# Kernel tuning notes

Measured on AMD Instinct MI355X. Metric: run time of the kernel, lower is better.

The kernel has to match this reference:

```python
import jax, jax.numpy as jnp
import numpy as np

D_MODEL = 1024
N_HEADS = 16
HEAD_DIM = D_MODEL // N_HEADS
D_FF = 4 * D_MODEL
SEQ = 2048
BATCH = 2
EPS = 1e-6


def setup_inputs() -> dict:
    key = jax.random.key(0)
    ks = jax.random.split(key, 8)
    s = 0.02
    return {
        "x": jax.random.normal(ks[0], (SEQ, BATCH, D_MODEL), dtype=jnp.float32),
        "g1": jnp.ones((D_MODEL,), dtype=jnp.float32),                # norm1 weight
        "g2": jnp.ones((D_MODEL,), dtype=jnp.float32),                # norm2 weight
        "Wq": jax.random.normal(ks[1], (N_HEADS, D_MODEL, HEAD_DIM), dtype=jnp.float32) * s,
        "Wk": jax.random.normal(ks[2], (N_HEADS, D_MODEL, HEAD_DIM), dtype=jnp.float32) * s,
        "Wv": jax.random.normal(ks[3], (N_HEADS, D_MODEL, HEAD_DIM), dtype=jnp.float32) * s,
        "Wo": jax.random.normal(ks[4], (D_MODEL, D_MODEL), dtype=jnp.float32) * s,
        "W1": jax.random.normal(ks[5], (D_MODEL, D_FF), dtype=jnp.float32) * s,
        "W2": jax.random.normal(ks[6], (D_FF, D_MODEL), dtype=jnp.float32) * s,
    }


def _rmsnorm(x, g):
    rms = jnp.sqrt(jnp.mean(x * x, axis=-1, keepdims=True) + EPS)
    return g * (x / rms)


def _block(x, g1, g2, Wq, Wk, Wv, Wo, W1, W2):
    S = x.shape[0]
    scale = HEAD_DIM ** -0.5
    # --- attention (pre-norm) ---
    h = _rmsnorm(x, g1)                              # (S, B, D)
    Q = jnp.einsum('sbd,hdk->bhsk', h, Wq)           # (B, H, S, K)
    K = jnp.einsum('sbd,hdk->bhsk', h, Wk)
    V = jnp.einsum('sbd,hdk->bhsk', h, Wv)
    scores = jnp.einsum('bhsk,bhtk->bhst', Q, K) * scale
    causal = jnp.tril(jnp.ones((S, S), dtype=bool))
    scores = jnp.where(causal, scores, -jnp.inf)
    attn = jax.nn.softmax(scores, axis=-1)
    ctx = jnp.einsum('bhst,bhtk->sbhk', attn, V)     # heads concatenated in order
    ctx = ctx.reshape(S, x.shape[1], D_MODEL)
    x = x + ctx @ Wo
    # --- FFN (pre-norm) ---
    h2 = _rmsnorm(x, g2)
    x = x + jax.nn.silu(h2 @ W1) @ W2
    return x


def reference(x, g1, g2, Wq, Wk, Wv, Wo, W1, W2):
    return _block(x, g1, g2, Wq, Wk, Wv, Wo, W1, W2)
```

## Files before the change

### kernel.cpp

```cpp
#include <hip/hip_runtime.h>

typedef unsigned short u16;
typedef __bf16 bf16x8 __attribute__((ext_vector_type(8)));
typedef u16 u16x8 __attribute__((ext_vector_type(8)));
typedef u16 u16x4 __attribute__((ext_vector_type(4)));
typedef float f32x4 __attribute__((ext_vector_type(4)));

__device__ __forceinline__ u16 f2bf(float f) {
    union { float f; unsigned int u; } x; x.f = f;
    unsigned int r = x.u + 0x7FFFu + ((x.u >> 16) & 1u);
    return (u16)(r >> 16);
}

__device__ __forceinline__ u16 f2bf_hw(float f) {
    union { __bf16 b; u16 u; } x; x.b = (__bf16)f; return x.u;
}

__device__ __forceinline__ void gload_lds16(const u16* g, u16* l) {
    __builtin_amdgcn_global_load_lds(
        (const __attribute__((address_space(1))) unsigned int*)g,
        (__attribute__((address_space(3))) unsigned int*)l, 16, 0, 0);
}


__global__ __launch_bounds__(256) void qkvT_k(
    const float* __restrict__ Wq, const float* __restrict__ Wk,
    const float* __restrict__ Wv, u16* __restrict__ out)
{
    __shared__ float T[64][65];
    const int d0 = blockIdx.x * 64;
    const int y = blockIdx.y;
    const int wsel = y >> 4, h = y & 15;
    const float* W = (wsel == 0) ? Wq : (wsel == 1) ? Wk : Wv;
    const float scale = (wsel == 0) ? 0.125f * 1.44269504088896f : 1.0f;
    const int tid = threadIdx.x;
    const int tr = tid >> 4;
    const int tc = (tid & 15) * 4;
    #pragma unroll
    for (int k = 0; k < 4; k++) {
        f32x4 v = *(const f32x4*)(W + (size_t)h * 65536 + (size_t)(d0 + 16 * k + tr) * 64 + tc);
        T[16 * k + tr][tc]     = v[0];
        T[16 * k + tr][tc + 1] = v[1];
        T[16 * k + tr][tc + 2] = v[2];
        T[16 * k + tr][tc + 3] = v[3];
    }
    __syncthreads();
    #pragma unroll
    for (int k = 0; k < 4; k++) {
        const int kk = 16 * k + tr;
        u16x4 o;
        #pragma unroll
        for (int i = 0; i < 4; i++) o[i] = f2bf(T[tc + i][kk] * scale);
        *(u16x4*)(out + (size_t)(wsel * 1024 + h * 64 + kk) * 1024 + d0 + tc) = o;
    }
}

__global__ __launch_bounds__(256) void transT_k(
    const float* __restrict__ in, u16* __restrict__ out, int R, int C)
{
    __shared__ float T[64][65];
    const int r0 = blockIdx.x * 64, c0 = blockIdx.y * 64;
    const int tid = threadIdx.x;
    const int tr = tid >> 4;
    const int tc = (tid & 15) * 4;
    #pragma unroll
    for (int k = 0; k < 4; k++) {
        f32x4 v = *(const f32x4*)(in + (size_t)(c0 + 16 * k + tr) * R + r0 + tc);
        T[16 * k + tr][tc]     = v[0];
        T[16 * k + tr][tc + 1] = v[1];
        T[16 * k + tr][tc + 2] = v[2];
        T[16 * k + tr][tc + 3] = v[3];
    }
    __syncthreads();
    #pragma unroll
    for (int k = 0; k < 4; k++) {
        const int rl = 16 * k + tr;
        u16x4 o;
        #pragma unroll
        for (int i = 0; i < 4; i++) o[i] = f2bf(T[tc + i][rl]);
        *(u16x4*)(out + (size_t)(r0 + rl) * C + c0 + tc) = o;
    }
}

__global__ __launch_bounds__(256) void vtrans_k(const u16* __restrict__ qkv, u16* __restrict__ vT)
{
    __shared__ u16 T[64][72];
    const int bh = blockIdx.x, b = bh >> 4, h = bh & 15;
    const int s0 = blockIdx.y * 64;
    const int tid = threadIdx.x;
    const int r = tid >> 2, c0 = (tid & 3) * 16;
    const u16* src = qkv + ((size_t)((s0 + r) * 2 + b)) * 3072 + 2048 + h * 64 + c0;
    *(u16x8*)&T[r][c0] = *(const u16x8*)src;
    *(u16x8*)&T[r][c0 + 8] = *(const u16x8*)(src + 8);
    __syncthreads();
    u16x8 o0, o1;
    #pragma unroll
    for (int i = 0; i < 8; i++) o0[i] = T[c0 + i][r];
    #pragma unroll
    for (int i = 0; i < 8; i++) o1[i] = T[c0 + 8 + i][r];
    u16* dst = vT + (size_t)(bh * 64 + r) * 2048 + s0 + c0;
    *(u16x8*)dst = o0;
    *(u16x8*)(dst + 8) = o1;
}

__global__ __launch_bounds__(256) void rmsnorm_k(
    const float* __restrict__ x, const float* __restrict__ g, u16* __restrict__ out)
{
    const int row = blockIdx.x;
    const int tid = threadIdx.x;
    const float* xr = x + (size_t)row * 1024;
    f32x4 v = *(const f32x4*)(xr + tid * 4);
    float ss = v[0] * v[0] + v[1] * v[1] + v[2] * v[2] + v[3] * v[3];
    #pragma unroll
    for (int off = 32; off > 0; off >>= 1) ss += __shfl_down(ss, off);
    __shared__ float red[4];
    if ((tid & 63) == 0) red[tid >> 6] = ss;
    __syncthreads();
    float sum = red[0] + red[1] + red[2] + red[3];
    float rinv = rsqrtf(sum * (1.0f / 1024.0f) + 1e-6f);
    f32x4 gv = *(const f32x4*)(g + tid * 4);
    u16x4 o;
    #pragma unroll
    for (int i = 0; i < 4; i++) o[i] = f2bf(v[i] * gv[i] * rinv);
    *(u16x4*)(out + (size_t)row * 1024 + tid * 4) = o;
}

__global__ __launch_bounds__(256) void addred_norm_k(
    const float* __restrict__ res, const float* __restrict__ p0,
    const float* __restrict__ p1, const float* __restrict__ g,
    float* __restrict__ xout, u16* __restrict__ hout)
{
    const int row = blockIdx.x;
    const int tid = threadIdx.x;
    const size_t base = (size_t)row * 1024 + tid * 4;
    f32x4 a = *(const f32x4*)(res + base);
    f32x4 b = *(const f32x4*)(p0 + base);
    f32x4 c = *(const f32x4*)(p1 + base);
    f32x4 o = a + b + c;
    *(f32x4*)(xout + base) = o;
    float ss = o[0] * o[0] + o[1] * o[1] + o[2] * o[2] + o[3] * o[3];
    #pragma unroll
    for (int off = 32; off > 0; off >>= 1) ss += __shfl_down(ss, off);
    __shared__ float red[4];
    if ((tid & 63) == 0) red[tid >> 6] = ss;
    __syncthreads();
    float sum = red[0] + red[1] + red[2] + red[3];
    float rinv = rsqrtf(sum * (1.0f / 1024.0f) + 1e-6f);
    f32x4 gv = *(const f32x4*)(g + tid * 4);
    u16x4 hv;
    #pragma unroll
    for (int i = 0; i < 4; i++) hv[i] = f2bf(o[i] * gv[i] * rinv);
    *(u16x4*)(hout + base) = hv;
}

__global__ __launch_bounds__(256) void addred_k(
    const float* __restrict__ res, const float* __restrict__ p0,
    const float* __restrict__ p1, float* __restrict__ out)
{
    int i = (blockIdx.x * 256 + threadIdx.x) * 4;
    f32x4 a = *(const f32x4*)(res + i);
    f32x4 b = *(const f32x4*)(p0 + i);
    f32x4 c = *(const f32x4*)(p1 + i);
    f32x4 o = a + b + c;
    *(f32x4*)(out + i) = o;
}

template <int MODE>
__global__ __launch_bounds__(256) void gemm_bt_k(
    const u16* __restrict__ A, const u16* __restrict__ BT,
    u16* __restrict__ outB, float* __restrict__ outF, const float* __restrict__ res,
    int M, int N, int K, int klen)
{
    __shared__ u16 As[128 * 64];
    __shared__ u16 Bs[128 * 64];
    const int tid = threadIdx.x;
    const int lane = tid & 63, w = tid >> 6;
    const int wm = w >> 1, wn = w & 1;
    const int quad = lane >> 4, l15 = lane & 15;
    const int bid = blockIdx.x + gridDim.x * blockIdx.y;
    const int bj = bid >> 3;
    const int m0 = ((bid & 7) * 4 + (bj & 3)) * 128;
    const int n0 = (bj >> 2) * 128;
    const int kbeg = blockIdx.z * klen;

    f32x4 acc[4][4] = {};

    const int srow = (w << 3) + (lane >> 3);
    const int swz = ((lane & 7) ^ (lane >> 3)) << 3;
    const u16* aA = A + (size_t)(m0 + srow) * K + kbeg + swz;
    const u16* aB = BT + (size_t)(n0 + srow) * K + kbeg + swz;
    u16* lA = As + w * 512;
    u16* lB = Bs + w * 512;
    const int rsw = (l15 & 7) << 3;

    for (int k0 = 0; k0 < klen; k0 += 64) {
        __syncthreads();
        #pragma unroll
        for (int c = 0; c < 4; c++)
            gload_lds16(aA + (size_t)(c * 32) * K + k0, lA + c * 2048);
        #pragma unroll
        for (int c = 0; c < 4; c++)
            gload_lds16(aB + (size_t)(c * 32) * K + k0, lB + c * 2048);
        __syncthreads();
        #pragma unroll
        for (int kh = 0; kh < 2; kh++) {
            const int cb = ((kh * 4 + quad) << 3);
            bf16x8 af[4], bfr[4];
            #pragma unroll
            for (int i = 0; i < 4; i++)
                af[i] = *(const bf16x8*)(As + (wm * 64 + i * 16 + l15) * 64 + (cb ^ rsw));
            #pragma unroll
            for (int j = 0; j < 4; j++)
                bfr[j] = *(const bf16x8*)(Bs + (wn * 64 + j * 16 + l15) * 64 + (cb ^ rsw));
            #pragma unroll
            for (int i = 0; i < 4; i++)
                #pragma unroll
                for (int j = 0; j < 4; j++)
                    acc[i][j] = __builtin_amdgcn_mfma_f32_16x16x32_bf16(af[i], bfr[j], acc[i][j], 0, 0, 0);
        }
    }

    float* outFz = (MODE == 3) ? outF + (size_t)blockIdx.z * M * N : outF;
    #pragma unroll
    for (int i = 0; i < 4; i++) {
        const int row = m0 + wm * 64 + i * 16 + quad * 4;
        #pragma unroll
        for (int j = 0; j < 4; j++) {
            const int col = n0 + wn * 64 + j * 16 + l15;
            #pragma unroll
            for (int r = 0; r < 4; r++) {
                const size_t idx = (size_t)(row + r) * N + col;
                float v = acc[i][j][r];
                if (MODE == 0) {
                    outB[idx] = f2bf(v);
                } else if (MODE == 1) {
                    outF[idx] = res[idx] + v;
                } else if (MODE == 2) {
                    outB[idx] = f2bf(v / (1.0f + __expf(-v)));
                } else {
                    outFz[idx] = v;
                }
            }
        }
    }
}

__global__ __launch_bounds__(256) void attn_k(const u16* __restrict__ qkv,
                                              const u16* __restrict__ vT,
                                              u16* __restrict__ ctx)
{
    const int bh = blockIdx.x;
    const int qt = 31 - (int)blockIdx.y;
    const int b = bh >> 4, h = bh & 15;
    const int q0 = qt * 64;
    const int tid = threadIdx.x;
    const int lane = tid & 63, w = tid >> 6;
    const int quad = lane >> 4, l15 = lane & 15;

    __shared__ u16 QP[64][72];
    __shared__ u16 Ks[2][4096];
    __shared__ u16 Vs[2][4096];

    {
        const int r = tid >> 2, c0 = (tid & 3) * 16;
        const u16* src = qkv + ((size_t)((q0 + r) * 2 + b)) * 3072 + h * 64 + c0;
        *(u16x8*)&QP[r][c0] = *(const u16x8*)(src);
        *(u16x8*)&QP[r][c0 + 8] = *(const u16x8*)(src + 8);
    }
    __syncthreads();

    const bf16x8 aq0 = *(const bf16x8*)&QP[16 * w + l15][quad * 8];
    const bf16x8 aq1 = *(const bf16x8*)&QP[16 * w + l15][32 + quad * 8];

    bf16x8 ones;
    #pragma unroll
    for (int i = 0; i < 8; i++) ones[i] = (__bf16)1.0f;

    const int kr = (w << 3) + (lane >> 3);
    const int swz = ((lane & 7) ^ (lane >> 3)) << 3;
    const int ldsoff = w * 512;
    const u16* kbase0 = qkv + ((size_t)(kr * 2 + b)) * 3072 + 1024 + h * 64 + swz;
    const u16* kbase1 = kbase0 + (size_t)32 * 2 * 3072;
    const u16* vrow0 = vT + (size_t)(bh * 64 + kr) * 2048 + swz;
    const u16* vrow1 = vrow0 + (size_t)32 * 2048;

    const int rsw = (l15 & 7) << 3;

    f32x4 o[4] = {};
    f32x4 accl = {};

    gload_lds16(kbase0, &Ks[0][0] + ldsoff);
    gload_lds16(kbase1, &Ks[0][0] + 2048 + ldsoff);
    gload_lds16(vrow0, &Vs[0][0] + ldsoff);
    gload_lds16(vrow1, &Vs[0][0] + 2048 + ldsoff);

    int cur = 0;
    for (int t0 = 0; t0 <= q0; t0 += 64) {
        __syncthreads();
        if (t0 + 64 <= q0) {
            const size_t go = (size_t)(t0 + 64) * 2 * 3072;
            u16* KB = &Ks[cur ^ 1][0];
            u16* VB = &Vs[cur ^ 1][0];
            gload_lds16(kbase0 + go, KB + ldsoff);
            gload_lds16(kbase1 + go, KB + 2048 + ldsoff);
            gload_lds16(vrow0 + (t0 + 64), VB + ldsoff);
            gload_lds16(vrow1 + (t0 + 64), VB + 2048 + ldsoff);
        }
        const u16* KB = &Ks[cur][0];
        const u16* VB = &Vs[cur][0];

        f32x4 s[4];
        #pragma unroll
        for (int j = 0; j < 4; j++) {
            const u16* kb = KB + (j * 16 + l15) * 64;
            bf16x8 bk0 = *(const bf16x8*)(kb + (((quad << 3) ^ rsw)));
            bf16x8 bk1 = *(const bf16x8*)(kb + ((((quad + 4) << 3) ^ rsw)));
            f32x4 c = {};
            c = __builtin_amdgcn_mfma_f32_16x16x32_bf16(aq0, bk0, c, 0, 0, 0);
            c = __builtin_amdgcn_mfma_f32_16x16x32_bf16(aq1, bk1, c, 0, 0, 0);
            s[j] = c;
        }

        if (t0 == q0) {
            #pragma unroll
            for (int j = 0; j < 4; j++)
                #pragma unroll
                for (int r = 0; r < 4; r++)
                    if ((j * 16 + l15) > (16 * w + quad * 4 + r)) s[j][r] = -1e30f;
        }

        #pragma unroll
        for (int j = 0; j < 4; j++)
            #pragma unroll
            for (int r = 0; r < 4; r++)
                QP[16 * w + quad * 4 + r][j * 16 + l15] = f2bf_hw(exp2f(s[j][r]));

        bf16x8 ap0 = *(const bf16x8*)&QP[16 * w + l15][quad * 8];
        bf16x8 ap1 = *(const bf16x8*)&QP[16 * w + l15][32 + quad * 8];
        accl = __builtin_amdgcn_mfma_f32_16x16x32_bf16(ap0, ones, accl, 0, 0, 0);
        accl = __builtin_amdgcn_mfma_f32_16x16x32_bf16(ap1, ones, accl, 0, 0, 0);
        #pragma unroll
        for (int j = 0; j < 4; j++) {
            const u16* vb = VB + (j * 16 + l15) * 64;
            bf16x8 bv0 = *(const bf16x8*)(vb + (((quad << 3) ^ rsw)));
            bf16x8 bv1 = *(const bf16x8*)(vb + ((((quad + 4) << 3) ^ rsw)));
            o[j] = __builtin_amdgcn_mfma_f32_16x16x32_bf16(ap0, bv0, o[j], 0, 0, 0);
            o[j] = __builtin_amdgcn_mfma_f32_16x16x32_bf16(ap1, bv1, o[j], 0, 0, 0);
        }
        cur ^= 1;
    }

    f32x4 linv;
    #pragma unroll
    for (int r = 0; r < 4; r++) linv[r] = 1.0f / accl[r];
    #pragma unroll
    for (int j = 0; j < 4; j++)
        #pragma unroll
        for (int r = 0; r < 4; r++) {
            int q = q0 + 16 * w + quad * 4 + r;
            int col = h * 64 + j * 16 + l15;
            ctx[((size_t)q * 2 + b) * 1024 + col] = f2bf_hw(o[j][r] * linv[r]);
        }
}

extern "C" void kernel_launch(void* const* d_in, const int* in_sizes, int n_in,
                              void* d_out, int out_size, void* d_ws, size_t ws_size,
                              hipStream_t stream)
{
    (void)in_sizes; (void)n_in; (void)out_size; (void)ws_size;
    const float* x  = (const float*)d_in[0];
    const float* g1 = (const float*)d_in[1];
    const float* g2 = (const float*)d_in[2];
    const float* Wq = (const float*)d_in[3];
    const float* Wk = (const float*)d_in[4];
    const float* Wv = (const float*)d_in[5];
    const float* Wo = (const float*)d_in[6];
    const float* W1 = (const float*)d_in[7];
    const float* W2 = (const float*)d_in[8];
    float* out = (float*)d_out;

    char* ws = (char*)d_ws;
    u16*   bqkvT = (u16*)(ws);
    u16*   woT   = (u16*)(ws + 6291456);
    u16*   w1T   = (u16*)(ws + 8388608);
    u16*   w2T   = (u16*)(ws + 16777216);
    u16*   h1    = (u16*)(ws + 25165824);
    u16*   qkvB  = (u16*)(ws + 33554432);
    u16*   ctxB  = (u16*)(ws + 58720256);
    float* xmid  = (float*)(ws + 67108864);
    u16*   h2    = (u16*)(ws + 83886080);
    u16*   actB  = (u16*)(ws + 92274688);
    u16*   vT    = (u16*)(ws + 25165824);
    float* part  = (float*)(ws + 25165824);
    float* partO = (float*)(ws + 92274688);

    qkvT_k<<<dim3(16, 48), 256, 0, stream>>>(Wq, Wk, Wv, bqkvT);
    transT_k<<<dim3(16, 16), 256, 0, stream>>>(Wo, woT, 1024, 1024);
    transT_k<<<dim3(64, 16), 256, 0, stream>>>(W1, w1T, 4096, 1024);
    transT_k<<<dim3(16, 64), 256, 0, stream>>>(W2, w2T, 1024, 4096);

    rmsnorm_k<<<4096, 256, 0, stream>>>(x, g1, h1);

    gemm_bt_k<0><<<dim3(24, 32), 256, 0, stream>>>(h1, bqkvT, qkvB, nullptr, nullptr,
                                                   4096, 3072, 1024, 1024);
    vtrans_k<<<dim3(32, 32), 256, 0, stream>>>(qkvB, vT);
    attn_k<<<dim3(32, 32), 256, 0, stream>>>(qkvB, vT, ctxB);

    gemm_bt_k<3><<<dim3(8, 32, 2), 256, 0, stream>>>(ctxB, woT, nullptr, partO, nullptr,
                                                     4096, 1024, 1024, 512);
    addred_norm_k<<<4096, 256, 0, stream>>>(x, partO, partO + 4096 * 1024, g2, xmid, h2);

    gemm_bt_k<2><<<dim3(32, 32), 256, 0, stream>>>(h2, w1T, actB, nullptr, nullptr,
                                                   4096, 4096, 1024, 1024);
    gemm_bt_k<3><<<dim3(8, 32, 2), 256, 0, stream>>>(actB, w2T, nullptr, part, nullptr,
                                                     4096, 1024, 4096, 2048);
    addred_k<<<4096 * 1024 / 1024, 256, 0, stream>>>(xmid, part, part + 4096 * 1024, out);
}
```

Baseline: 335.4 us.

## Double-buffer GEMM LDS tiles and use hardware bf16 conversion in epilogue

The GEMM now keeps two LDS buffers for the A and B tiles. It prefetches the next K-slice with global_load_lds while the MFMAs run on the current slice, which cuts the loop to one barrier per iteration. The aim is to overlap global-to-LDS transfer with compute instead of stalling on every tile. The epilogue also switches to the hardware float-to-bf16 conversion and computes SiLU with exp2 and a reciprocal intrinsic. The cost is twice the LDS per block, which may lower occupancy, and slightly different rounding and approximation in the epilogue.

```diff
diff --git a/kernel.cpp b/kernel.cpp
--- a/kernel.cpp
+++ b/kernel.cpp
@@ -171,8 +171,8 @@
     u16* __restrict__ outB, float* __restrict__ outF, const float* __restrict__ res,
     int M, int N, int K, int klen)
 {
-    __shared__ u16 As[128 * 64];
-    __shared__ u16 Bs[128 * 64];
+    __shared__ u16 As[2][128 * 64];
+    __shared__ u16 Bs[2][128 * 64];
     const int tid = threadIdx.x;
     const int lane = tid & 63, w = tid >> 6;
     const int wm = w >> 1, wn = w & 1;
@@ -189,35 +189,44 @@
     const int swz = ((lane & 7) ^ (lane >> 3)) << 3;
     const u16* aA = A + (size_t)(m0 + srow) * K + kbeg + swz;
     const u16* aB = BT + (size_t)(n0 + srow) * K + kbeg + swz;
-    u16* lA = As + w * 512;
-    u16* lB = Bs + w * 512;
+    const int wo = w * 512;
     const int rsw = (l15 & 7) << 3;
 
+    #pragma unroll
+    for (int c = 0; c < 4; c++) {
+        gload_lds16(aA + (size_t)(c * 32) * K, &As[0][0] + c * 2048 + wo);
+        gload_lds16(aB + (size_t)(c * 32) * K, &Bs[0][0] + c * 2048 + wo);
+    }
+
+    int cur = 0;
     for (int k0 = 0; k0 < klen; k0 += 64) {
         __syncthreads();
-        #pragma unroll
-        for (int c = 0; c < 4; c++)
-            gload_lds16(aA + (size_t)(c * 32) * K + k0, lA + c * 2048);
-        #pragma unroll
-        for (int c = 0; c < 4; c++)
-            gload_lds16(aB + (size_t)(c * 32) * K + k0, lB + c * 2048);
-        __syncthreads();
+        if (k0 + 64 < klen) {
+            #pragma unroll
+            for (int c = 0; c < 4; c++) {
+                gload_lds16(aA + (size_t)(c * 32) * K + k0 + 64, &As[cur ^ 1][0] + c * 2048 + wo);
+                gload_lds16(aB + (size_t)(c * 32) * K + k0 + 64, &Bs[cur ^ 1][0] + c * 2048 + wo);
+            }
+        }
+        const u16* AB = &As[cur][0];
+        const u16* BB = &Bs[cur][0];
         #pragma unroll
         for (int kh = 0; kh < 2; kh++) {
             const int cb = ((kh * 4 + quad) << 3);
             bf16x8 af[4], bfr[4];
             #pragma unroll
             for (int i = 0; i < 4; i++)
-                af[i] = *(const bf16x8*)(As + (wm * 64 + i * 16 + l15) * 64 + (cb ^ rsw));
+                af[i] = *(const bf16x8*)(AB + (wm * 64 + i * 16 + l15) * 64 + (cb ^ rsw));
             #pragma unroll
             for (int j = 0; j < 4; j++)
-                bfr[j] = *(const bf16x8*)(Bs + (wn * 64 + j * 16 + l15) * 64 + (cb ^ rsw));
+                bfr[j] = *(const bf16x8*)(BB + (wn * 64 + j * 16 + l15) * 64 + (cb ^ rsw));
             #pragma unroll
             for (int i = 0; i < 4; i++)
                 #pragma unroll
                 for (int j = 0; j < 4; j++)
                     acc[i][j] = __builtin_amdgcn_mfma_f32_16x16x32_bf16(af[i], bfr[j], acc[i][j], 0, 0, 0);
         }
+        cur ^= 1;
     }
 
     float* outFz = (MODE == 3) ? outF + (size_t)blockIdx.z * M * N : outF;
@@ -232,11 +241,12 @@
                 const size_t idx = (size_t)(row + r) * N + col;
                 float v = acc[i][j][r];
                 if (MODE == 0) {
-                    outB[idx] = f2bf(v);
+                    outB[idx] = f2bf_hw(v);
                 } else if (MODE == 1) {
                     outF[idx] = res[idx] + v;
                 } else if (MODE == 2) {
-                    outB[idx] = f2bf(v / (1.0f + __expf(-v)));
+                    float e = exp2f(v * -1.44269504088896f);
+                    outB[idx] = f2bf_hw(v * __builtin_amdgcn_rcpf(1.0f + e));
                 } else {
                     outFz[idx] = v;
                 }
```

Measured after the change: 326.8 us. 2.6% less time.
